# Optimization experiments

Hardware: AMD Instinct MI355X
Metric: run time of the kernel (lower is better)

Reference implementation:

```python
import jax, jax.numpy as jnp
import numpy as np

B, C, H, W = 16, 256, 32, 32
NUM_LAYERS = 30
OUT = 16  # sqrt(out_channels)
EPS = 1e-5


def setup_inputs() -> dict:
    key = jax.random.key(0)
    k1, k2, k3 = jax.random.split(key, 3)
    x = jax.random.normal(k1, (B, C, H, W), dtype=jnp.float32)
    # delta_t ~ small positive values (module inits ~N(0.01, 0.005))
    delta_t = jax.random.uniform(k2, (NUM_LAYERS, 1), dtype=jnp.float32) * 0.02
    matrices = jax.random.normal(k3, (NUM_LAYERS, 1, 1, OUT, OUT), dtype=jnp.float32) * 0.1
    gamma = jnp.ones((H * W,), dtype=jnp.float32)   # BatchNorm2d weight, oc = i*i = H*W
    beta = jnp.zeros((H * W,), dtype=jnp.float32)   # BatchNorm2d bias
    return {"x": x, "delta_t": delta_t, "matrices": matrices, "gamma": gamma, "beta": beta}


def _bn_relu6(z, gamma, beta):
    # training-mode BatchNorm2d over channel axis 1 (channels = H*W), then ReLU6
    mean = jnp.mean(z, axis=(0, 2, 3), keepdims=True)
    var = jnp.mean(jnp.square(z - mean), axis=(0, 2, 3), keepdims=True)  # biased var
    zhat = (z - mean) * jax.lax.rsqrt(var + EPS)
    g = gamma.reshape(1, -1, 1, 1)
    b = beta.reshape(1, -1, 1, 1)
    return jnp.clip(zhat * g + b, 0.0, 6.0)


def reference(x, delta_t, matrices, gamma, beta):
    b, c, h, w = x.shape
    hw = h * w
    # feature_reshape: [B,C,H,W] -> [B,HW,C] -> [B,HW,out,out] (inn == out branch)
    x1 = x.reshape(b, c, hw).transpose(0, 2, 1).reshape(b, hw, OUT, OUT)
    dt = jnp.clip(delta_t, 0.0, 6.0)[:, 0]  # relu6(delta_t), shape [L]

    def step(y0, params):
        m, dtl = params  # m: [1,1,out,out] broadcasts elementwise against x1
        dydt = -y0 + _bn_relu6(y0 + m * x1, gamma, beta)
        return y0 + dtl * dydt, None

    y0, _ = jax.lax.scan(step, x1, (matrices, dt))
    # (y0 + x1): [B, HW, out, out] -> view [B,H,W,out*out] -> permute to [B,out*out,H,W]
    y = (y0 + x1).reshape(b, h, w, OUT * OUT).transpose(0, 3, 1, 2)
    return y
```

## Files before the change

### kernel.cpp

```cpp
#include <hip/hip_runtime.h>

typedef float v2f __attribute__((ext_vector_type(2)));
typedef float v4f __attribute__((ext_vector_type(4)));

#define HW      1024
#define NROWS   4096
#define NLAYERS 30
#define TPB     256

static __device__ __forceinline__ v2f pk_fma(v2f a, v2f b, v2f c) {
    v2f d; asm("v_pk_fma_f32 %0, %1, %2, %3" : "=v"(d) : "v"(a), "v"(b), "v"(c));
    return d;
}
static __device__ __forceinline__ v2f pk_add(v2f a, v2f b) {
    v2f d; asm("v_pk_add_f32 %0, %1, %2" : "=v"(d) : "v"(a), "v"(b));
    return d;
}
static __device__ __forceinline__ v2f pk_mul(v2f a, v2f b) {
    v2f d; asm("v_pk_mul_f32 %0, %1, %2" : "=v"(d) : "v"(a), "v"(b));
    return d;
}

template <int CTRL, int RMASK>
__device__ __forceinline__ float dpp_add(float x) {
    int t = __builtin_amdgcn_update_dpp(0, __builtin_bit_cast(int, x),
                                        CTRL, RMASK, 0xf, true);
    return x + __builtin_bit_cast(float, t);
}
__device__ __forceinline__ float wave_sum64(float x) {
    x = dpp_add<0x111, 0xf>(x);
    x = dpp_add<0x112, 0xf>(x);
    x = dpp_add<0x114, 0xf>(x);
    x = dpp_add<0x118, 0xf>(x);
    x = dpp_add<0x142, 0xa>(x);
    x = dpp_add<0x143, 0xc>(x);
    return x;
}

__global__ __launch_bounds__(TPB) void txp64(const float* __restrict__ src,
                                             float* __restrict__ dst,
                                             int M, int N) {
    __shared__ float tile[64][65];
    const int n0 = blockIdx.x * 64;
    const int m0 = blockIdx.y * 64;
    const int tx = threadIdx.x & 63;
    const int ty = threadIdx.x >> 6;
#pragma unroll
    for (int i = 0; i < 16; ++i) {
        const int r = ty + 4 * i;
        tile[r][tx] = src[(size_t)(m0 + r) * N + n0 + tx];
    }
    __syncthreads();
#pragma unroll
    for (int i = 0; i < 16; ++i) {
        const int r = ty + 4 * i;
        dst[(size_t)(n0 + r) * M + m0 + tx] = tile[tx][r];
    }
}

__global__ __launch_bounds__(TPB, 4) void ode_row(
    float* ws, const float* __restrict__ delta_t,
    const float* __restrict__ matrices, const float* __restrict__ gamma,
    const float* __restrict__ beta) {

    const int p    = blockIdx.x;
    const int t    = threadIdx.x;
    const int wid  = t >> 6;
    const int lane = t & 63;
    const int c0   = (4 * t) & 255;

    __shared__ __align__(16) v2f red[2][4];

    float* row = ws + (size_t)p * NROWS;

    v2f x1[8], y[8], z[8];
#pragma unroll
    for (int k = 0; k < 4; ++k) {
        const v4f q4 = *(const v4f*)(row + 4 * t + 1024 * k);
        x1[2 * k]     = (v2f){q4.x, q4.y};
        x1[2 * k + 1] = (v2f){q4.z, q4.w};
        y[2 * k]     = x1[2 * k];
        y[2 * k + 1] = x1[2 * k + 1];
    }

    const float gp = gamma[p];
    const float bp = beta[p];

    {
        const v4f m4 = *(const v4f*)(matrices + c0);
        const v2f mA = {m4.x, m4.y}, mB = {m4.z, m4.w};
        v2f s = {0.f, 0.f}, q = {0.f, 0.f};
#pragma unroll
        for (int k = 0; k < 4; ++k) {
            z[2 * k] = pk_fma(mA, x1[2 * k], y[2 * k]);
            s = pk_add(s, z[2 * k]);
            q = pk_fma(z[2 * k], z[2 * k], q);
            z[2 * k + 1] = pk_fma(mB, x1[2 * k + 1], y[2 * k + 1]);
            s = pk_add(s, z[2 * k + 1]);
            q = pk_fma(z[2 * k + 1], z[2 * k + 1], q);
        }
        const float ss = wave_sum64(s.x + s.y);
        const float qq = wave_sum64(q.x + q.y);
        if (lane == 63) red[0][wid] = (v2f){ss, qq};
    }

    v4f   m_cur4 = *(const v4f*)(matrices + 256 + c0);
    float dt_cur = delta_t[0];
    float dt_nxt = delta_t[1];
    __syncthreads();

    for (int k = 0; k < NLAYERS - 1; ++k) {
        const int k2 = (k + 2 < NLAYERS) ? k + 2 : NLAYERS - 1;
        const v4f   m_nxt4 = *(const v4f*)(matrices + k2 * 256 + c0);
        const float dt_nn  = delta_t[k2];

        const int par = k & 1;
        const v4f r0 = *(const v4f*)&red[par][0];
        const v4f r1 = *(const v4f*)&red[par][2];
        const float S = (r0.x + r0.z) + (r1.x + r1.z);
        const float Q = (r0.y + r0.w) + (r1.y + r1.w);

        const float dtk  = __builtin_amdgcn_fmed3f(dt_cur, 0.0f, 6.0f);
        const float mean = S * (1.0f / 4096.0f);
        const float var  = fmaf(-mean, mean, Q * (1.0f / 4096.0f));
        const float rstd = rsqrtf(var + 1e-5f);
        const float g    = gp * rstd;
        const float b    = fmaf(-mean, g, bp);
        const v2f g2 = {g, g}, b2 = {b, b};
        const v2f dt2 = {dtk, dtk};
        const v2f om2 = {1.0f - dtk, 1.0f - dtk};
        const v2f mA = {m_cur4.x, m_cur4.y}, mB = {m_cur4.z, m_cur4.w};

        v2f s = {0.f, 0.f}, q = {0.f, 0.f};
#pragma unroll
        for (int j = 0; j < 8; ++j) {
            v2f a = pk_fma(z[j], g2, b2);
            a.x = __builtin_amdgcn_fmed3f(a.x, 0.0f, 6.0f);
            a.y = __builtin_amdgcn_fmed3f(a.y, 0.0f, 6.0f);
            y[j] = pk_mul(om2, y[j]);
            y[j] = pk_fma(dt2, a, y[j]);
            z[j] = pk_fma((j & 1) ? mB : mA, x1[j], y[j]);
            s = pk_add(s, z[j]);
            q = pk_fma(z[j], z[j], q);
        }
        const float ss = wave_sum64(s.x + s.y);
        const float qq = wave_sum64(q.x + q.y);
        if (lane == 63) red[par ^ 1][wid] = (v2f){ss, qq};

        m_cur4 = m_nxt4; dt_cur = dt_nxt; dt_nxt = dt_nn;
        __syncthreads();
    }

    {
        const v4f r0 = *(const v4f*)&red[(NLAYERS - 1) & 1][0];
        const v4f r1 = *(const v4f*)&red[(NLAYERS - 1) & 1][2];
        const float S = (r0.x + r0.z) + (r1.x + r1.z);
        const float Q = (r0.y + r0.w) + (r1.y + r1.w);

        const float dtk  = __builtin_amdgcn_fmed3f(dt_cur, 0.0f, 6.0f);
        const float mean = S * (1.0f / 4096.0f);
        const float var  = fmaf(-mean, mean, Q * (1.0f / 4096.0f));
        const float rstd = rsqrtf(var + 1e-5f);
        const float g    = gp * rstd;
        const float b    = fmaf(-mean, g, bp);
        const v2f g2 = {g, g}, b2 = {b, b};
        const v2f dt2 = {dtk, dtk};
        const v2f om2 = {1.0f - dtk, 1.0f - dtk};

#pragma unroll
        for (int k = 0; k < 4; ++k) {
            v2f o0, o1;
#pragma unroll
            for (int h = 0; h < 2; ++h) {
                const int j = 2 * k + h;
                v2f a = pk_fma(z[j], g2, b2);
                a.x = __builtin_amdgcn_fmed3f(a.x, 0.0f, 6.0f);
                a.y = __builtin_amdgcn_fmed3f(a.y, 0.0f, 6.0f);
                v2f yy = pk_mul(om2, y[j]);
                yy = pk_fma(dt2, a, yy);
                const v2f o = pk_add(yy, x1[j]);
                if (h == 0) o0 = o; else o1 = o;
            }
            v4f o4; o4.x = o0.x; o4.y = o0.y; o4.z = o1.x; o4.w = o1.y;
            *(v4f*)(row + 4 * t + 1024 * k) = o4;
        }
    }
}

__global__ __launch_bounds__(TPB) void ode_fused(const float* __restrict__ x,
                                                 const float* __restrict__ delta_t,
                                                 const float* __restrict__ matrices,
                                                 const float* __restrict__ gamma,
                                                 const float* __restrict__ beta,
                                                 float* __restrict__ out) {
    const int bid = blockIdx.x;
    const int p   = ((bid & 7) << 7) | (bid >> 3);
    const int t   = threadIdx.x;

    __shared__ float smat[(NLAYERS + 1) * 256];
    __shared__ float sdt[NLAYERS];
    __shared__ __align__(16) v2f red[2][4];

#pragma unroll
    for (int i = 0; i < NLAYERS; ++i)
        smat[i * 256 + t] = matrices[i * 256 + t];
    if (t < NLAYERS)
        sdt[t] = __builtin_amdgcn_fmed3f(delta_t[t], 0.0f, 6.0f);

    v2f x1[8], y[8];
#pragma unroll
    for (int k = 0; k < 8; ++k) {
        x1[k].x = x[(size_t)(t + 512 * k) * HW + p];
        x1[k].y = x[(size_t)(t + 512 * k + 256) * HW + p];
        y[k] = x1[k];
    }

    const float gp   = gamma[p];
    const float bp   = beta[p];
    const int   wid  = t >> 6;
    const int   lane = t & 63;

    __syncthreads();
    float m_cur = smat[t];

    for (int l = 0; l < NLAYERS; ++l) {
        const float dtl = sdt[l];
        const v2f m2    = {m_cur, m_cur};
        const v2f dt2   = {dtl, dtl};
        const v2f om2   = {1.0f - dtl, 1.0f - dtl};

        v2f z[8];
        v2f sA = {0.f, 0.f}, sB = {0.f, 0.f};
        v2f qA = {0.f, 0.f}, qB = {0.f, 0.f};
#pragma unroll
        for (int k = 0; k < 8; k += 2) {
            z[k]     = __builtin_elementwise_fma(m2, x1[k], y[k]);
            z[k + 1] = __builtin_elementwise_fma(m2, x1[k + 1], y[k + 1]);
            sA += z[k];
            sB += z[k + 1];
            qA = __builtin_elementwise_fma(z[k], z[k], qA);
            qB = __builtin_elementwise_fma(z[k + 1], z[k + 1], qB);
        }
#pragma unroll
        for (int k = 0; k < 8; ++k) y[k] *= om2;

        const v2f sv = sA + sB;
        const v2f qv = qA + qB;
        float s = wave_sum64(sv.x + sv.y);
        float q = wave_sum64(qv.x + qv.y);

        const int par = l & 1;
        if (lane == 63) { v2f w; w.x = s; w.y = q; red[par][wid] = w; }
        m_cur = smat[(l + 1) * 256 + t];
        __syncthreads();

        const float4 r0 = *(const float4*)&red[par][0];
        const float4 r1 = *(const float4*)&red[par][2];
        const float S  = (r0.x + r0.z) + (r1.x + r1.z);
        const float S2 = (r0.y + r0.w) + (r1.y + r1.w);

        const float mean = S * (1.0f / 4096.0f);
        const float var  = fmaf(-mean, mean, S2 * (1.0f / 4096.0f));
        const float rstd = rsqrtf(var + 1e-5f);
        const float g    = gp * rstd;
        const float bb   = fmaf(-mean, g, bp);
        const v2f g2 = {g, g}, b2 = {bb, bb};
        const v2f z0 = {0.f, 0.f}, s6 = {6.f, 6.f};
#pragma unroll
        for (int k = 0; k < 8; ++k) {
            v2f a = __builtin_elementwise_fma(z[k], g2, b2);
            a = __builtin_elementwise_max(a, z0);
            a = __builtin_elementwise_min(a, s6);
            y[k] = __builtin_elementwise_fma(dt2, a, y[k]);
        }
    }

#pragma unroll
    for (int k = 0; k < 8; ++k) {
        out[(size_t)(t + 512 * k) * HW + p]       = y[k].x + x1[k].x;
        out[(size_t)(t + 512 * k + 256) * HW + p] = y[k].y + x1[k].y;
    }
}

extern "C" void kernel_launch(void* const* d_in, const int* in_sizes, int n_in,
                              void* d_out, int out_size, void* d_ws, size_t ws_size,
                              hipStream_t stream) {
    const float* x        = (const float*)d_in[0];
    const float* delta_t  = (const float*)d_in[1];
    const float* matrices = (const float*)d_in[2];
    const float* gamma    = (const float*)d_in[3];
    const float* beta     = (const float*)d_in[4];
    float* out = (float*)d_out;

    const size_t need = (size_t)HW * NROWS * sizeof(float);
    if (d_ws != nullptr && ws_size >= need) {
        float* ws = (float*)d_ws;
        txp64<<<dim3(HW / 64, NROWS / 64), dim3(TPB), 0, stream>>>(x, ws, NROWS, HW);
        ode_row<<<dim3(HW), dim3(TPB), 0, stream>>>(ws, delta_t, matrices, gamma, beta);
        txp64<<<dim3(NROWS / 64, HW / 64), dim3(TPB), 0, stream>>>(ws, out, HW, NROWS);
    } else {
        ode_fused<<<dim3(HW), dim3(TPB), 0, stream>>>(x, delta_t, matrices, gamma, beta, out);
    }
}
```

Before: 120.0 us.

## Process each BN channel with a single wave, removing block-level reductions

```diff
diff --git a/kernel.cpp b/kernel.cpp
--- a/kernel.cpp
+++ b/kernel.cpp
@@ -36,6 +36,10 @@
     x = dpp_add<0x143, 0xc>(x);
     return x;
 }
+__device__ __forceinline__ float bcast63(float x) {
+    return __builtin_bit_cast(float,
+        __builtin_amdgcn_readlane(__builtin_bit_cast(int, x), 63));
+}
 
 __global__ __launch_bounds__(TPB) void txp64(const float* __restrict__ src,
                                              float* __restrict__ dst,
@@ -58,69 +62,61 @@
     }
 }
 
-__global__ __launch_bounds__(TPB, 4) void ode_row(
+__global__ __launch_bounds__(64, 1) void ode_row1w(
     float* ws, const float* __restrict__ delta_t,
     const float* __restrict__ matrices, const float* __restrict__ gamma,
     const float* __restrict__ beta) {
 
     const int p    = blockIdx.x;
-    const int t    = threadIdx.x;
-    const int wid  = t >> 6;
-    const int lane = t & 63;
-    const int c0   = (4 * t) & 255;
-
-    __shared__ __align__(16) v2f red[2][4];
-
+    const int lane = threadIdx.x;
     float* row = ws + (size_t)p * NROWS;
 
-    v2f x1[8], y[8], z[8];
-#pragma unroll
-    for (int k = 0; k < 4; ++k) {
-        const v4f q4 = *(const v4f*)(row + 4 * t + 1024 * k);
-        x1[2 * k]     = (v2f){q4.x, q4.y};
-        x1[2 * k + 1] = (v2f){q4.z, q4.w};
-        y[2 * k]     = x1[2 * k];
-        y[2 * k + 1] = x1[2 * k + 1];
+    v2f x1[32], y[32], z[32];
+#pragma unroll
+    for (int j = 0; j < 16; ++j) {
+        const v4f q4 = *(const v4f*)(row + 4 * lane + 256 * j);
+        x1[2 * j]     = (v2f){q4.x, q4.y};
+        x1[2 * j + 1] = (v2f){q4.z, q4.w};
+        y[2 * j]     = x1[2 * j];
+        y[2 * j + 1] = x1[2 * j + 1];
     }
 
     const float gp = gamma[p];
     const float bp = beta[p];
 
+    v2f sa[4], qa[4];
+
     {
-        const v4f m4 = *(const v4f*)(matrices + c0);
+        const v4f m4 = *(const v4f*)(matrices + 4 * lane);
         const v2f mA = {m4.x, m4.y}, mB = {m4.z, m4.w};
-        v2f s = {0.f, 0.f}, q = {0.f, 0.f};
-#pragma unroll
-        for (int k = 0; k < 4; ++k) {
-            z[2 * k] = pk_fma(mA, x1[2 * k], y[2 * k]);
-            s = pk_add(s, z[2 * k]);
-            q = pk_fma(z[2 * k], z[2 * k], q);
-            z[2 * k + 1] = pk_fma(mB, x1[2 * k + 1], y[2 * k + 1]);
-            s = pk_add(s, z[2 * k + 1]);
-            q = pk_fma(z[2 * k + 1], z[2 * k + 1], q);
-        }
-        const float ss = wave_sum64(s.x + s.y);
-        const float qq = wave_sum64(q.x + q.y);
-        if (lane == 63) red[0][wid] = (v2f){ss, qq};
-    }
-
-    v4f   m_cur4 = *(const v4f*)(matrices + 256 + c0);
-    float dt_cur = delta_t[0];
-    float dt_nxt = delta_t[1];
-    __syncthreads();
+#pragma unroll
+        for (int r = 0; r < 4; ++r) { sa[r] = (v2f){0.f, 0.f}; qa[r] = (v2f){0.f, 0.f}; }
+#pragma unroll
+        for (int j = 0; j < 16; ++j) {
+            z[2 * j]     = pk_fma(mA, x1[2 * j], y[2 * j]);
+            z[2 * j + 1] = pk_fma(mB, x1[2 * j + 1], y[2 * j + 1]);
+            sa[j & 3] = pk_add(sa[j & 3], z[2 * j]);
+            qa[j & 3] = pk_fma(z[2 * j], z[2 * j], qa[j & 3]);
+            sa[(j + 2) & 3] = pk_add(sa[(j + 2) & 3], z[2 * j + 1]);
+            qa[(j + 2) & 3] = pk_fma(z[2 * j + 1], z[2 * j + 1], qa[(j + 2) & 3]);
+        }
+    }
+
+    v4f   mq  = *(const v4f*)(matrices + 256 + 4 * lane);
+    float dtc = delta_t[0];
+    float dtn = delta_t[1];
 
     for (int k = 0; k < NLAYERS - 1; ++k) {
         const int k2 = (k + 2 < NLAYERS) ? k + 2 : NLAYERS - 1;
-        const v4f   m_nxt4 = *(const v4f*)(matrices + k2 * 256 + c0);
-        const float dt_nn  = delta_t[k2];
-
-        const int par = k & 1;
-        const v4f r0 = *(const v4f*)&red[par][0];
-        const v4f r1 = *(const v4f*)&red[par][2];
-        const float S = (r0.x + r0.z) + (r1.x + r1.z);
-        const float Q = (r0.y + r0.w) + (r1.y + r1.w);
-
-        const float dtk  = __builtin_amdgcn_fmed3f(dt_cur, 0.0f, 6.0f);
+        const v4f   mq_n  = *(const v4f*)(matrices + k2 * 256 + 4 * lane);
+        const float dt_nn = delta_t[k2];
+
+        const v2f sv = pk_add(pk_add(sa[0], sa[1]), pk_add(sa[2], sa[3]));
+        const v2f qv = pk_add(pk_add(qa[0], qa[1]), pk_add(qa[2], qa[3]));
+        const float S = bcast63(wave_sum64(sv.x + sv.y));
+        const float Q = bcast63(wave_sum64(qv.x + qv.y));
+
+        const float dtk  = __builtin_amdgcn_fmed3f(dtc, 0.0f, 6.0f);
         const float mean = S * (1.0f / 4096.0f);
         const float var  = fmaf(-mean, mean, Q * (1.0f / 4096.0f));
         const float rstd = rsqrtf(var + 1e-5f);
@@ -129,35 +125,37 @@
         const v2f g2 = {g, g}, b2 = {b, b};
         const v2f dt2 = {dtk, dtk};
         const v2f om2 = {1.0f - dtk, 1.0f - dtk};
-        const v2f mA = {m_cur4.x, m_cur4.y}, mB = {m_cur4.z, m_cur4.w};
-
-        v2f s = {0.f, 0.f}, q = {0.f, 0.f};
-#pragma unroll
-        for (int j = 0; j < 8; ++j) {
-            v2f a = pk_fma(z[j], g2, b2);
-            a.x = __builtin_amdgcn_fmed3f(a.x, 0.0f, 6.0f);
-            a.y = __builtin_amdgcn_fmed3f(a.y, 0.0f, 6.0f);
-            y[j] = pk_mul(om2, y[j]);
-            y[j] = pk_fma(dt2, a, y[j]);
-            z[j] = pk_fma((j & 1) ? mB : mA, x1[j], y[j]);
-            s = pk_add(s, z[j]);
-            q = pk_fma(z[j], z[j], q);
-        }
-        const float ss = wave_sum64(s.x + s.y);
-        const float qq = wave_sum64(q.x + q.y);
-        if (lane == 63) red[par ^ 1][wid] = (v2f){ss, qq};
-
-        m_cur4 = m_nxt4; dt_cur = dt_nxt; dt_nxt = dt_nn;
-        __syncthreads();
+        const v2f mA = {mq.x, mq.y}, mB = {mq.z, mq.w};
+
+#pragma unroll
+        for (int r = 0; r < 4; ++r) { sa[r] = (v2f){0.f, 0.f}; qa[r] = (v2f){0.f, 0.f}; }
+
+#pragma unroll
+        for (int j = 0; j < 16; ++j) {
+#pragma unroll
+            for (int h = 0; h < 2; ++h) {
+                const int e = 2 * j + h;
+                v2f a = pk_fma(z[e], g2, b2);
+                a.x = __builtin_amdgcn_fmed3f(a.x, 0.0f, 6.0f);
+                a.y = __builtin_amdgcn_fmed3f(a.y, 0.0f, 6.0f);
+                v2f yy = pk_mul(om2, y[e]);
+                y[e] = pk_fma(dt2, a, yy);
+                z[e] = pk_fma(h ? mB : mA, x1[e], y[e]);
+                sa[(j + 2 * h) & 3] = pk_add(sa[(j + 2 * h) & 3], z[e]);
+                qa[(j + 2 * h) & 3] = pk_fma(z[e], z[e], qa[(j + 2 * h) & 3]);
+            }
+        }
+
+        mq = mq_n; dtc = dtn; dtn = dt_nn;
     }
 
     {
-        const v4f r0 = *(const v4f*)&red[(NLAYERS - 1) & 1][0];
-        const v4f r1 = *(const v4f*)&red[(NLAYERS - 1) & 1][2];
-        const float S = (r0.x + r0.z) + (r1.x + r1.z);
-        const float Q = (r0.y + r0.w) + (r1.y + r1.w);
-
-        const float dtk  = __builtin_amdgcn_fmed3f(dt_cur, 0.0f, 6.0f);
+        const v2f sv = pk_add(pk_add(sa[0], sa[1]), pk_add(sa[2], sa[3]));
+        const v2f qv = pk_add(pk_add(qa[0], qa[1]), pk_add(qa[2], qa[3]));
+        const float S = bcast63(wave_sum64(sv.x + sv.y));
+        const float Q = bcast63(wave_sum64(qv.x + qv.y));
+
+        const float dtk  = __builtin_amdgcn_fmed3f(dtc, 0.0f, 6.0f);
         const float mean = S * (1.0f / 4096.0f);
         const float var  = fmaf(-mean, mean, Q * (1.0f / 4096.0f));
         const float rstd = rsqrtf(var + 1e-5f);
@@ -168,21 +166,21 @@
         const v2f om2 = {1.0f - dtk, 1.0f - dtk};
 
 #pragma unroll
-        for (int k = 0; k < 4; ++k) {
+        for (int j = 0; j < 16; ++j) {
             v2f o0, o1;
 #pragma unroll
             for (int h = 0; h < 2; ++h) {
-                const int j = 2 * k + h;
-                v2f a = pk_fma(z[j], g2, b2);
+                const int e = 2 * j + h;
+                v2f a = pk_fma(z[e], g2, b2);
                 a.x = __builtin_amdgcn_fmed3f(a.x, 0.0f, 6.0f);
                 a.y = __builtin_amdgcn_fmed3f(a.y, 0.0f, 6.0f);
-                v2f yy = pk_mul(om2, y[j]);
+                v2f yy = pk_mul(om2, y[e]);
                 yy = pk_fma(dt2, a, yy);
-                const v2f o = pk_add(yy, x1[j]);
+                const v2f o = pk_add(yy, x1[e]);
                 if (h == 0) o0 = o; else o1 = o;
             }
             v4f o4; o4.x = o0.x; o4.y = o0.y; o4.z = o1.x; o4.w = o1.y;
-            *(v4f*)(row + 4 * t + 1024 * k) = o4;
+            *(v4f*)(row + 4 * lane + 256 * j) = o4;
         }
     }
 }
@@ -296,7 +294,7 @@
     if (d_ws != nullptr && ws_size >= need) {
         float* ws = (float*)d_ws;
         txp64<<<dim3(HW / 64, NROWS / 64), dim3(TPB), 0, stream>>>(x, ws, NROWS, HW);
-        ode_row<<<dim3(HW), dim3(TPB), 0, stream>>>(ws, delta_t, matrices, gamma, beta);
+        ode_row1w<<<dim3(HW), dim3(64), 0, stream>>>(ws, delta_t, matrices, gamma, beta);
         txp64<<<dim3(NROWS / 64, HW / 64), dim3(TPB), 0, stream>>>(ws, out, HW, NROWS);
     } else {
         ode_fused<<<dim3(HW), dim3(TPB), 0, stream>>>(x, delta_t, matrices, gamma, beta, out);
```

Result: faster. 111.7 us (-6.9%).
